# Kernel optimization log

Measured on AMD Instinct MI355X. Metric: run time of the kernel, lower is better.

The kernel has to match this reference:

```python
import jax, jax.numpy as jnp
import numpy as np


def _conv(x, w):
    # x: (B, Cin, 3, 3), w: (Cout, Cin, 3, 3), SAME padding
    return jax.lax.conv_general_dilated(
        x, w, window_strides=(1, 1), padding='SAME',
        dimension_numbers=('NCHW', 'OIHW', 'NCHW'))


def _convlstm_dir(x_seq, w, b, reverse):
    # x_seq: (T, B, Cin, 3, 3); w: (4H, Cin+H, 3, 3); b: (4H,)
    T, B = x_seq.shape[0], x_seq.shape[1]
    H = w.shape[0] // 4
    h0 = jnp.zeros((B, H, 3, 3), x_seq.dtype)
    c0 = jnp.zeros_like(h0)

    def step(carry, x_t):
        h, c = carry
        z = _conv(jnp.concatenate([x_t, h], axis=1), w) + b[None, :, None, None]
        i, f, o, g = jnp.split(z, 4, axis=1)
        c = jax.nn.sigmoid(f) * c + jax.nn.sigmoid(i) * jnp.tanh(g)
        h = jax.nn.sigmoid(o) * jnp.tanh(c)
        return (h, c), h

    _, hs = jax.lax.scan(step, (h0, c0), x_seq, reverse=reverse)
    return hs  # (T, B, H, 3, 3), aligned to input time order


def setup_inputs() -> dict:
    key = jax.random.key(0)
    ks = jax.random.split(key, 8)
    B, T, C, H, NC = 64, 128, 256, 128, 7
    s0 = 1.0 / np.sqrt((C + H) * 9)
    s1 = 1.0 / np.sqrt((H + H) * 9)
    sf = 1.0 / np.sqrt(H * 9)
    return {
        'x': jax.random.normal(ks[0], (B, T, C, 3, 3), jnp.float32),
        'w_f0': jax.random.normal(ks[1], (4 * H, C + H, 3, 3), jnp.float32) * s0,
        'b_f0': jnp.zeros((4 * H,), jnp.float32),
        'w_b0': jax.random.normal(ks[2], (4 * H, C + H, 3, 3), jnp.float32) * s0,
        'b_b0': jnp.zeros((4 * H,), jnp.float32),
        'w_f1': jax.random.normal(ks[3], (4 * H, 2 * H, 3, 3), jnp.float32) * s1,
        'b_f1': jnp.zeros((4 * H,), jnp.float32),
        'w_b1': jax.random.normal(ks[4], (4 * H, 2 * H, 3, 3), jnp.float32) * s1,
        'b_b1': jnp.zeros((4 * H,), jnp.float32),
        'fc_w': jax.random.normal(ks[5], (NC, H * 9), jnp.float32) * sf,
        'fc_b': jnp.zeros((NC,), jnp.float32),
    }


def reference(x, w_f0, b_f0, w_b0, b_b0, w_f1, b_f1, w_b1, b_b1, fc_w, fc_b):
    # x: (B, T, C, 3, 3)
    xs = jnp.transpose(x, (1, 0, 2, 3, 4))  # (T, B, C, 3, 3)
    # layer 0: bidirectional, outputs summed
    h = _convlstm_dir(xs, w_f0, b_f0, False) + _convlstm_dir(xs, w_b0, b_b0, True)
    # layer 1
    h = _convlstm_dir(h, w_f1, b_f1, False) + _convlstm_dir(h, w_b1, b_b1, True)
    out = jnp.transpose(h, (1, 0, 2, 3, 4))  # (B, T, H, 3, 3)
    B, T = out.shape[0], out.shape[1]
    out = out.reshape(B, T, -1)  # (B, T, H*9)
    return out @ fc_w.T + fc_b  # (B, T, num_classes)
```

## Files before the change

kernel.cpp:

```cpp
#include <hip/hip_runtime.h>
#include <hip/hip_fp16.h>

typedef _Float16 half8 __attribute__((ext_vector_type(8)));
typedef _Float16 half4v __attribute__((ext_vector_type(4)));
typedef float floatx4 __attribute__((ext_vector_type(4)));

#define T_    128
#define B_    64
#define HCH   128
#define NQ    4608
#define KH    1152
#define NROWS 8192

__device__ __forceinline__ float sigm(float x){ return 1.0f/(1.0f + __expf(-x)); }

__device__ __forceinline__ void gll16(const _Float16* g, const _Float16* l){
  __builtin_amdgcn_global_load_lds(
      (const __attribute__((address_space(1))) unsigned int*)g,
      (__attribute__((address_space(3))) unsigned int*)l, 16, 0, 0);
}

__global__ void k_cast_f16(const float* __restrict__ src, _Float16* __restrict__ dst, int n4){
  int i = blockIdx.x*blockDim.x + threadIdx.x;
  if (i >= n4) return;
  float4 v = ((const float4*)src)[i];
  half4v h;
  h[0] = (_Float16)v.x; h[1] = (_Float16)v.y; h[2] = (_Float16)v.z; h[3] = (_Float16)v.w;
  ((half4v*)dst)[i] = h;
}

__global__ void k_pack_w2(const float* __restrict__ w, _Float16* __restrict__ Wx,
                          _Float16* __restrict__ Wh, int Cx, int total){
  int idx = blockIdx.x*256 + threadIdx.x;
  if (idx >= total) return;
  int Kx = Cx*9;
  int nWx = NQ*Kx;
  int n, kk, ci;
  _Float16* dst;
  bool pad = false;
  if (idx < nWx) { n = idx / Kx; kk = idx % Kx; ci = kk/9; dst = Wx + idx; }
  else {
    int e = idx - nWx;
    n = e / KH; kk = e % KH; ci = Cx + kk/9; dst = Wh + e;
    pad = (n >= NQ);
  }
  float val = 0.0f;
  if (!pad) {
    int ch = n/36, g = (n%36)/9, p = n%9, q = kk%9;
    int kr = q/3 - p/3 + 1, kc = q%3 - p%3 + 1;
    if (kr>=0 && kr<3 && kc>=0 && kc<3)
      val = w[(((g*HCH+ch)*(Cx+HCH) + ci)*3 + kr)*3 + kc];
  }
  *dst = (_Float16)val;
}

__global__ void k_pack_bias(const float* __restrict__ b0f, const float* __restrict__ b0b,
                            const float* __restrict__ b1f, const float* __restrict__ b1b,
                            float* __restrict__ outb){
  int idx = blockIdx.x*256 + threadIdx.x;
  if (idx >= 4*NQ) return;
  int li = idx / NQ, n = idx % NQ;
  const float* src = (li==0)?b0f : (li==1)?b0b : (li==2)?b1f : b1b;
  int ch = n/36, g = (n%36)/9;
  outb[idx] = src[g*HCH + ch];
}

__global__ __launch_bounds__(256) void k_gemm(
    const _Float16* __restrict__ A, const _Float16* __restrict__ Bt,
    _Float16* __restrict__ Co, const float* __restrict__ biasArr, int K)
{
  __shared__ _Float16 As[128*32];
  __shared__ _Float16 Bs[128*32];
  int flat = blockIdx.x;
  int cpx  = gridDim.x >> 3;
  int swz  = (flat & 7)*cpx + (flat >> 3);
  int dir  = swz / (64*36);
  int rem  = swz % (64*36);
  size_t m0 = (size_t)(rem / 36) * 128;
  size_t n0 = (size_t)(rem % 36) * 128;
  const _Float16* Bd = Bt + (size_t)dir*NQ*K;
  _Float16*       Cd = Co + (size_t)dir*NROWS*NQ;
  const float* bias  = biasArr + dir*NQ;

  int tid = threadIdx.x;
  int w = tid >> 6, l = tid & 63;
  int wm = w >> 1, wn = w & 1;
  int lr = l & 15, lk = l >> 4;
  int sr = tid >> 2, sc = tid & 3;

  floatx4 acc[4][4] = {};
  for (int kt = 0; kt < K; kt += 32) {
    __syncthreads();
    {
      int r = sr;       int cg = sc ^ ((r>>1)&3);
      gll16(A  + (m0 + r)*K + kt + cg*8, As + r*32 + sc*8);
      r = sr + 64;      cg = sc ^ ((r>>1)&3);
      gll16(A  + (m0 + r)*K + kt + cg*8, As + r*32 + sc*8);
      r = sr;           cg = sc ^ ((r>>1)&3);
      gll16(Bd + (n0 + r)*K + kt + cg*8, Bs + r*32 + sc*8);
      r = sr + 64;      cg = sc ^ ((r>>1)&3);
      gll16(Bd + (n0 + r)*K + kt + cg*8, Bs + r*32 + sc*8);
    }
    __syncthreads();
    half8 a[4], b[4];
    #pragma unroll
    for (int mi=0; mi<4; ++mi){
      int row = wm*64 + mi*16 + lr;
      int sl  = lk ^ ((row>>1)&3);
      a[mi] = *(const half8*)(As + row*32 + sl*8);
    }
    #pragma unroll
    for (int ni=0; ni<4; ++ni){
      int row = wn*64 + ni*16 + lr;
      int sl  = lk ^ ((row>>1)&3);
      b[ni] = *(const half8*)(Bs + row*32 + sl*8);
    }
    #pragma unroll
    for (int mi=0; mi<4; ++mi)
      #pragma unroll
      for (int ni=0; ni<4; ++ni)
        acc[mi][ni] = __builtin_amdgcn_mfma_f32_16x16x32_f16(a[mi], b[ni], acc[mi][ni], 0,0,0);
  }
  #pragma unroll
  for (int mi=0; mi<4; ++mi)
    #pragma unroll
    for (int ni=0; ni<4; ++ni)
      #pragma unroll
      for (int j=0; j<4; ++j) {
        size_t m = m0 + wm*64 + mi*16 + lk*4 + j;
        size_t n = n0 + wn*64 + ni*16 + lr;
        Cd[m*NQ + n] = (_Float16)(acc[mi][ni][j] + bias[n]);
      }
}

__global__ __launch_bounds__(256) void k_step(
    const _Float16* __restrict__ Wh,
    const _Float16* __restrict__ Zx,
    const _Float16* __restrict__ Hin,
    _Float16* __restrict__ Hout,
    float* __restrict__ Cst,
    _Float16* __restrict__ HS,
    int s)
{
  __shared__ float red[4][64][52];
  int bid = blockIdx.x;
  int d = bid >> 7, ch = bid & 127;
  int t = d ? (T_-1-s) : s;
  int tid = threadIdx.x, w = tid >> 6, l = tid & 63;
  int lr = l & 15, lk = l >> 4;
  const _Float16* hb = Hin + (size_t)d*B_*KH;
  const _Float16* wb = Wh  + (size_t)d*4620*KH + (size_t)(ch*36)*KH;

  floatx4 acc[4][3] = {};
  #pragma unroll
  for (int ki = 0; ki < 9; ++ki) {
    int k = w*288 + ki*32 + lk*8;
    half8 a[4], b[3];
    #pragma unroll
    for (int mi=0; mi<4; ++mi) a[mi] = *(const half8*)(hb + (size_t)(mi*16+lr)*KH + k);
    #pragma unroll
    for (int ni=0; ni<3; ++ni) b[ni] = *(const half8*)(wb + (size_t)(ni*16+lr)*KH + k);
    #pragma unroll
    for (int mi=0; mi<4; ++mi)
      #pragma unroll
      for (int ni=0; ni<3; ++ni)
        acc[mi][ni] = __builtin_amdgcn_mfma_f32_16x16x32_f16(a[mi], b[ni], acc[mi][ni], 0,0,0);
  }
  #pragma unroll
  for (int mi=0; mi<4; ++mi)
    #pragma unroll
    for (int ni=0; ni<3; ++ni)
      #pragma unroll
      for (int j=0; j<4; ++j)
        red[w][mi*16 + lk*4 + j][ni*16 + lr] = acc[mi][ni][j];
  __syncthreads();

  for (int pi = tid; pi < 576; pi += 256) {
    int row = pi/9, p = pi%9;
    const _Float16* zr = Zx + (size_t)d*NROWS*NQ + (size_t)(row*T_ + t)*NQ + ch*36;
    float zv[4];
    #pragma unroll
    for (int g=0; g<4; ++g) {
      int c0 = g*9+p;
      zv[g] = red[0][row][c0]+red[1][row][c0]+red[2][row][c0]+red[3][row][c0] + (float)zr[c0];
    }
    size_t ii = (size_t)d*B_*KH + (size_t)row*KH + ch*9 + p;
    float co = Cst[ii];
    float cn = sigm(zv[1])*co + sigm(zv[0])*tanhf(zv[3]);
    float h  = sigm(zv[2])*tanhf(cn);
    Cst[ii]  = cn;
    Hout[ii] = (_Float16)h;
    HS[(size_t)((d*T_ + t)*B_ + row)*KH + ch*9 + p] = (_Float16)h;
  }
}

__global__ void k_pack_A1(const _Float16* __restrict__ hs, _Float16* __restrict__ A1, int nchunks){
  int i = blockIdx.x*256 + threadIdx.x;
  if (i >= nchunks) return;
  int r  = i / (KH/8);
  int kc = i % (KH/8);
  int b = r / T_, t = r % T_;
  half8 xv = ((const half8*)(hs + (size_t)(t*B_ + b)*KH))[kc];
  half8 yv = ((const half8*)(hs + (size_t)((T_ + t)*B_ + b)*KH))[kc];
  half8 o;
  #pragma unroll
  for (int e=0; e<8; ++e) o[e] = (_Float16)((float)xv[e] + (float)yv[e]);
  ((half8*)A1)[i] = o;
}

__global__ __launch_bounds__(64) void k_fc(const _Float16* __restrict__ hs,
                                           const float* __restrict__ fw,
                                           const float* __restrict__ fb,
                                           float* __restrict__ out){
  int r = blockIdx.x;
  int b = r / T_, t = r % T_;
  int l = threadIdx.x;
  const _Float16* ha = hs + (size_t)(t*B_ + b)*KH;
  const _Float16* hc = hs + (size_t)((T_ + t)*B_ + b)*KH;
  float accv[7] = {0,0,0,0,0,0,0};
  for (int k=l; k<KH; k+=64){
    float h = (float)ha[k] + (float)hc[k];
    #pragma unroll
    for (int nc=0; nc<7; ++nc) accv[nc] += h * fw[nc*KH + k];
  }
  #pragma unroll
  for (int nc=0; nc<7; ++nc){
    float v = accv[nc];
    for (int off=32; off; off>>=1) v += __shfl_down(v, off, 64);
    if (l==0) out[(size_t)r*7 + nc] = v + fb[nc];
  }
}

extern "C" void kernel_launch(void* const* d_in, const int* in_sizes, int n_in,
                              void* d_out, int out_size, void* d_ws, size_t ws_size,
                              hipStream_t stream)
{
  const float* x    = (const float*)d_in[0];
  const float* w_f0 = (const float*)d_in[1];
  const float* b_f0 = (const float*)d_in[2];
  const float* w_b0 = (const float*)d_in[3];
  const float* b_b0 = (const float*)d_in[4];
  const float* w_f1 = (const float*)d_in[5];
  const float* b_f1 = (const float*)d_in[6];
  const float* w_b1 = (const float*)d_in[7];
  const float* b_b1 = (const float*)d_in[8];
  const float* fc_w = (const float*)d_in[9];
  const float* fc_b = (const float*)d_in[10];
  float* out = (float*)d_out;

  char* base = (char*)d_ws;
  const size_t TOTAL = 256112640;
  if (ws_size < TOTAL) {
    (void)hipMemsetAsync(d_out, 0x7F, (size_t)out_size*4, stream);
    return;
  }
  _Float16* A0   = (_Float16*)(base);
  _Float16* A1   = (_Float16*)(base);
  _Float16* WxT1 = (_Float16*)(base + 18874368);
  _Float16* WxT0 = (_Float16*)(base + 40108032);
  _Float16* hs0  = (_Float16*)(base + 40108032);
  _Float16* hs1  = (_Float16*)(base + 40108032);
  _Float16* Zx   = (_Float16*)(base + 82575360);
  _Float16* WhT0 = (_Float16*)(base + 233570304);
  _Float16* WhT1 = (_Float16*)(base + 233570304);
  float*    biasn= (float*)   (base + 254859264);
  _Float16* Hb   = (_Float16*)(base + 254932992);
  float*    Cb   = (float*)   (base + 255522816);

  int tot0 = NQ*2304 + 4620*KH;
  int tot1 = NQ*1152 + 4620*KH;

  k_cast_f16<<<18874368/4/256, 256, 0, stream>>>(x, A0, 18874368/4);
  k_pack_w2<<<(tot0+255)/256,256,0,stream>>>(w_f0, WxT0,                   WhT0,           256, tot0);
  k_pack_w2<<<(tot0+255)/256,256,0,stream>>>(w_b0, WxT0 + (size_t)NQ*2304, WhT0 + 4620*KH, 256, tot0);
  k_pack_bias<<<(4*NQ+255)/256,256,0,stream>>>(b_f0,b_b0,b_f1,b_b1, biasn);

  (void)hipMemsetAsync(Hb, 0, 589824, stream);
  (void)hipMemsetAsync(Cb, 0, 589824, stream);
  k_gemm<<<4608, 256, 0, stream>>>(A0, WxT0, Zx, biasn, 2304);
  for (int s=0; s<T_; ++s){
    _Float16* hin  = Hb + (size_t)(s&1)*(2*B_*KH);
    _Float16* hout = Hb + (size_t)((s&1)^1)*(2*B_*KH);
    k_step<<<256,256,0,stream>>>(WhT0, Zx, hin, hout, Cb, hs0, s);
  }

  k_pack_w2<<<(tot1+255)/256,256,0,stream>>>(w_f1, WxT1,                   WhT1,           128, tot1);
  k_pack_w2<<<(tot1+255)/256,256,0,stream>>>(w_b1, WxT1 + (size_t)NQ*1152, WhT1 + 4620*KH, 128, tot1);
  k_pack_A1<<<(NROWS*KH/8+255)/256,256,0,stream>>>(hs0, A1, NROWS*KH/8);

  (void)hipMemsetAsync(Hb, 0, 589824, stream);
  (void)hipMemsetAsync(Cb, 0, 589824, stream);
  k_gemm<<<4608, 256, 0, stream>>>(A1, WxT1, Zx, biasn + 2*NQ, 1152);
  for (int s=0; s<T_; ++s){
    _Float16* hin  = Hb + (size_t)(s&1)*(2*B_*KH);
    _Float16* hout = Hb + (size_t)((s&1)^1)*(2*B_*KH);
    k_step<<<256,256,0,stream>>>(WhT1, Zx, hin, hout, Cb, hs1, s);
  }

  k_fc<<<NROWS, 64, 0, stream>>>(hs1, fc_w, fc_b, out);
}
```

Before: 4.460 ms.

## Fuse per-timestep step launches into persistent scan kernel with grid barrier

Replaces 128 per-timestep k_step launches per layer with one persistent k_scan kernel of 256 blocks that synchronises through a global atomic barrier. Each block loads its slice of the recurrent weights into LDS once, with an XOR swizzle to avoid bank conflicts, and keeps the cell state in registers. Each wave now handles 16 batch rows over the full K instead of splitting K across waves. The gate columns are reordered to an interleaved i,f,o,g layout so each thread reads its four gates with one vector load. This removes launch overhead and repeated weight reloads, but depends on all 256 blocks being co-resident, and the spin barrier has a timeout escape that could break correctness.

```diff
diff --git a/kernel.cpp b/kernel.cpp
--- a/kernel.cpp
+++ b/kernel.cpp
@@ -46,7 +46,7 @@
   }
   float val = 0.0f;
   if (!pad) {
-    int ch = n/36, g = (n%36)/9, p = n%9, q = kk%9;
+    int ch = n/36, r = n%36, p = r>>2, g = r&3, q = kk%9;
     int kr = q/3 - p/3 + 1, kc = q%3 - p%3 + 1;
     if (kr>=0 && kr<3 && kc>=0 && kc<3)
       val = w[(((g*HCH+ch)*(Cx+HCH) + ci)*3 + kr)*3 + kc];
@@ -61,7 +61,7 @@
   if (idx >= 4*NQ) return;
   int li = idx / NQ, n = idx % NQ;
   const float* src = (li==0)?b0f : (li==1)?b0b : (li==2)?b1f : b1b;
-  int ch = n/36, g = (n%36)/9;
+  int ch = n/36, g = (n%36)&3;
   outb[idx] = src[g*HCH + ch];
 }
 
@@ -133,64 +133,105 @@
       }
 }
 
-__global__ __launch_bounds__(256) void k_step(
+__global__ __launch_bounds__(256) void k_scan(
     const _Float16* __restrict__ Wh,
     const _Float16* __restrict__ Zx,
-    const _Float16* __restrict__ Hin,
-    _Float16* __restrict__ Hout,
-    float* __restrict__ Cst,
+    _Float16* __restrict__ Hb,
     _Float16* __restrict__ HS,
-    int s)
+    unsigned* bar)
 {
-  __shared__ float red[4][64][52];
+  __shared__ _Float16 wlds[48*KH];
+  __shared__ float red[4][16][48];
   int bid = blockIdx.x;
   int d = bid >> 7, ch = bid & 127;
-  int t = d ? (T_-1-s) : s;
   int tid = threadIdx.x, w = tid >> 6, l = tid & 63;
   int lr = l & 15, lk = l >> 4;
-  const _Float16* hb = Hin + (size_t)d*B_*KH;
-  const _Float16* wb = Wh  + (size_t)d*4620*KH + (size_t)(ch*36)*KH;
-
-  floatx4 acc[4][3] = {};
-  #pragma unroll
-  for (int ki = 0; ki < 9; ++ki) {
-    int k = w*288 + ki*32 + lk*8;
-    half8 a[4], b[3];
-    #pragma unroll
-    for (int mi=0; mi<4; ++mi) a[mi] = *(const half8*)(hb + (size_t)(mi*16+lr)*KH + k);
-    #pragma unroll
-    for (int ni=0; ni<3; ++ni) b[ni] = *(const half8*)(wb + (size_t)(ni*16+lr)*KH + k);
-    #pragma unroll
-    for (int mi=0; mi<4; ++mi)
+  const _Float16* wb  = Wh + (size_t)d*4620*KH + (size_t)(ch*36)*KH;
+  const _Float16* zxd = Zx + (size_t)d*NROWS*NQ + ch*36;
+
+  for (int idx = tid; idx < 48*144; idx += 256) {
+    int row = idx/144, c = idx%144;
+    half8 v = *(const half8*)(wb + (size_t)row*KH + c*8);
+    *(half8*)(wlds + (size_t)row*KH + (size_t)((c ^ (row&7))*8)) = v;
+  }
+  __syncthreads();
+
+  float cst0 = 0.f, cst1 = 0.f, cst2 = 0.f;
+
+  for (int s = 0; s < T_; ++s) {
+    int t = d ? (T_-1-s) : s;
+    int par = s & 1;
+    const _Float16* hin  = Hb + (size_t)(par*2 + d)*B_*KH;
+    _Float16*       hout = Hb + (size_t)(((par^1)*2) + d)*B_*KH;
+    _Float16*       hsd  = HS + (size_t)((d*T_ + t)*B_)*KH + ch*9;
+
+    half4v zp0 = {}, zp1 = {}, zp2 = {};
+    {
+      int pi = l;        int row = pi/9, p = pi%9;
+      zp0 = *(const half4v*)(zxd + (size_t)((w*16+row)*T_ + t)*NQ + p*4);
+      pi = l + 64;       row = pi/9; p = pi%9;
+      zp1 = *(const half4v*)(zxd + (size_t)((w*16+row)*T_ + t)*NQ + p*4);
+      pi = l + 128;
+      if (pi < 144) { row = pi/9; p = pi%9;
+        zp2 = *(const half4v*)(zxd + (size_t)((w*16+row)*T_ + t)*NQ + p*4); }
+    }
+
+    floatx4 acc[3] = {};
+    #pragma unroll 6
+    for (int ki = 0; ki < 36; ++ki) {
+      half8 a = *(const half8*)(hin + (size_t)(w*16+lr)*KH + ki*32 + lk*8);
       #pragma unroll
-      for (int ni=0; ni<3; ++ni)
-        acc[mi][ni] = __builtin_amdgcn_mfma_f32_16x16x32_f16(a[mi], b[ni], acc[mi][ni], 0,0,0);
-  }
-  #pragma unroll
-  for (int mi=0; mi<4; ++mi)
+      for (int ni = 0; ni < 3; ++ni) {
+        int row = ni*16 + lr;
+        int cc = (ki*4 + lk) ^ (row & 7);
+        half8 b = *(const half8*)(wlds + (size_t)row*KH + cc*8);
+        acc[ni] = __builtin_amdgcn_mfma_f32_16x16x32_f16(a, b, acc[ni], 0,0,0);
+      }
+    }
     #pragma unroll
     for (int ni=0; ni<3; ++ni)
       #pragma unroll
       for (int j=0; j<4; ++j)
-        red[w][mi*16 + lk*4 + j][ni*16 + lr] = acc[mi][ni][j];
-  __syncthreads();
-
-  for (int pi = tid; pi < 576; pi += 256) {
-    int row = pi/9, p = pi%9;
-    const _Float16* zr = Zx + (size_t)d*NROWS*NQ + (size_t)(row*T_ + t)*NQ + ch*36;
-    float zv[4];
-    #pragma unroll
-    for (int g=0; g<4; ++g) {
-      int c0 = g*9+p;
-      zv[g] = red[0][row][c0]+red[1][row][c0]+red[2][row][c0]+red[3][row][c0] + (float)zr[c0];
-    }
-    size_t ii = (size_t)d*B_*KH + (size_t)row*KH + ch*9 + p;
-    float co = Cst[ii];
-    float cn = sigm(zv[1])*co + sigm(zv[0])*tanhf(zv[3]);
-    float h  = sigm(zv[2])*tanhf(cn);
-    Cst[ii]  = cn;
-    Hout[ii] = (_Float16)h;
-    HS[(size_t)((d*T_ + t)*B_ + row)*KH + ch*9 + p] = (_Float16)h;
+        red[w][lk*4+j][ni*16+lr] = acc[ni][j];
+
+    #pragma unroll
+    for (int ii=0; ii<3; ++ii) {
+      int pi = l + ii*64;
+      if (pi < 144) {
+        int row = pi/9, p = pi%9;
+        int brow = w*16 + row;
+        floatx4 rv = *(floatx4*)&red[w][row][p*4];
+        half4v z = (ii==0)?zp0:((ii==1)?zp1:zp2);
+        float zi = (float)z[0] + rv[0];
+        float zf = (float)z[1] + rv[1];
+        float zo = (float)z[2] + rv[2];
+        float zg = (float)z[3] + rv[3];
+        float& cc = (ii==0)?cst0:((ii==1)?cst1:cst2);
+        float cn = sigm(zf)*cc + sigm(zi)*tanhf(zg);
+        float h  = sigm(zo)*tanhf(cn);
+        cc = cn;
+        _Float16 hh = (_Float16)h;
+        hout[(size_t)brow*KH + ch*9 + p] = hh;
+        hsd[(size_t)brow*KH + p] = hh;
+      }
+    }
+
+    __syncthreads();
+    if (tid == 0) {
+      unsigned g = __hip_atomic_load(bar+1, __ATOMIC_RELAXED, __HIP_MEMORY_SCOPE_AGENT);
+      unsigned old = __hip_atomic_fetch_add(bar, 1u, __ATOMIC_ACQ_REL, __HIP_MEMORY_SCOPE_AGENT);
+      if (old == 255u) {
+        __hip_atomic_store(bar, 0u, __ATOMIC_RELAXED, __HIP_MEMORY_SCOPE_AGENT);
+        __hip_atomic_store(bar+1, g+1u, __ATOMIC_RELEASE, __HIP_MEMORY_SCOPE_AGENT);
+      } else {
+        int tries = 0;
+        while (__hip_atomic_load(bar+1, __ATOMIC_ACQUIRE, __HIP_MEMORY_SCOPE_AGENT) == g) {
+          __builtin_amdgcn_s_sleep(2);
+          if (++tries > (1<<22)) break;
+        }
+      }
+    }
+    __syncthreads();
   }
 }
 
@@ -265,7 +306,7 @@
   _Float16* WhT1 = (_Float16*)(base + 233570304);
   float*    biasn= (float*)   (base + 254859264);
   _Float16* Hb   = (_Float16*)(base + 254932992);
-  float*    Cb   = (float*)   (base + 255522816);
+  unsigned* bar  = (unsigned*)(base + 255522816);
 
   int tot0 = NQ*2304 + 4620*KH;
   int tot1 = NQ*1152 + 4620*KH;
@@ -276,26 +317,18 @@
   k_pack_bias<<<(4*NQ+255)/256,256,0,stream>>>(b_f0,b_b0,b_f1,b_b1, biasn);
 
   (void)hipMemsetAsync(Hb, 0, 589824, stream);
-  (void)hipMemsetAsync(Cb, 0, 589824, stream);
+  (void)hipMemsetAsync(bar, 0, 16, stream);
   k_gemm<<<4608, 256, 0, stream>>>(A0, WxT0, Zx, biasn, 2304);
-  for (int s=0; s<T_; ++s){
-    _Float16* hin  = Hb + (size_t)(s&1)*(2*B_*KH);
-    _Float16* hout = Hb + (size_t)((s&1)^1)*(2*B_*KH);
-    k_step<<<256,256,0,stream>>>(WhT0, Zx, hin, hout, Cb, hs0, s);
-  }
+  k_scan<<<256, 256, 0, stream>>>(WhT0, Zx, Hb, hs0, bar);
 
   k_pack_w2<<<(tot1+255)/256,256,0,stream>>>(w_f1, WxT1,                   WhT1,           128, tot1);
   k_pack_w2<<<(tot1+255)/256,256,0,stream>>>(w_b1, WxT1 + (size_t)NQ*1152, WhT1 + 4620*KH, 128, tot1);
   k_pack_A1<<<(NROWS*KH/8+255)/256,256,0,stream>>>(hs0, A1, NROWS*KH/8);
 
   (void)hipMemsetAsync(Hb, 0, 589824, stream);
-  (void)hipMemsetAsync(Cb, 0, 589824, stream);
+  (void)hipMemsetAsync(bar, 0, 16, stream);
   k_gemm<<<4608, 256, 0, stream>>>(A1, WxT1, Zx, biasn + 2*NQ, 1152);
-  for (int s=0; s<T_; ++s){
-    _Float16* hin  = Hb + (size_t)(s&1)*(2*B_*KH);
-    _Float16* hout = Hb + (size_t)((s&1)^1)*(2*B_*KH);
-    k_step<<<256,256,0,stream>>>(WhT1, Zx, hin, hout, Cb, hs1, s);
-  }
+  k_scan<<<256, 256, 0, stream>>>(WhT1, Zx, Hb, hs1, bar);
 
   k_fc<<<NROWS, 64, 0, stream>>>(hs1, fc_w, fc_b, out);
 }
```

Result: slower. 8.083 ms (+81.2%).
